# Kernel tuning notes

Measured on AMD Instinct MI355X. Metric: run time of the kernel, lower is better.

Reference implementation:

```python
import jax, jax.numpy as jnp
import numpy as np

N_NODES = 50000
N_EDGES = 1200000
IN_DIM = 128
EDGE_DIM = 64
EMBED_DIM = 64
NUM_HEADS = 8


def segment_softmax(logits, segment_ids, num_segments):
    # numerically stable softmax over segments (receivers)
    mx = jax.ops.segment_max(logits, segment_ids, num_segments)
    e = jnp.exp(logits - mx[segment_ids])
    denom = jax.ops.segment_sum(e, segment_ids, num_segments)
    return e / denom[segment_ids]


def mish(x):
    return x * jnp.tanh(jax.nn.softplus(x))


def setup_inputs() -> dict:
    key = jax.random.key(0)
    ks = jax.random.split(key, 8)
    node_features = jax.random.normal(ks[0], (N_NODES, IN_DIM), dtype=jnp.float32)
    edge_features = jax.random.normal(ks[1], (N_EDGES, EDGE_DIM), dtype=jnp.float32)
    global_features = jax.random.normal(ks[2], (32,), dtype=jnp.float32)
    senders = jax.random.randint(ks[3], (N_EDGES,), 0, N_NODES, dtype=jnp.int32)
    receivers = jax.random.randint(ks[4], (N_EDGES,), 0, N_NODES, dtype=jnp.int32)
    W_kernel = jax.random.normal(ks[5], (IN_DIM, EMBED_DIM), dtype=jnp.float32) * (2.0 / (IN_DIM + EMBED_DIM)) ** 0.5
    W_bias = jnp.zeros((EMBED_DIM,), dtype=jnp.float32)
    We_kernel = jax.random.normal(ks[6], (EDGE_DIM, EMBED_DIM), dtype=jnp.float32) * (2.0 / (EDGE_DIM + EMBED_DIM)) ** 0.5
    We_bias = jnp.zeros((EMBED_DIM,), dtype=jnp.float32)
    a = jax.random.normal(ks[7], (NUM_HEADS, EMBED_DIM // NUM_HEADS), dtype=jnp.float32) * (2.0 / (NUM_HEADS + EMBED_DIM // NUM_HEADS)) ** 0.5
    return dict(node_features=node_features, edge_features=edge_features,
                global_features=global_features, senders=senders, receivers=receivers,
                W_kernel=W_kernel, W_bias=W_bias, We_kernel=We_kernel, We_bias=We_bias, a=a)


def reference(node_features, edge_features, global_features, senders, receivers,
              W_kernel, W_bias, We_kernel, We_bias, a):
    num_nodes = node_features.shape[0]
    H, D = a.shape  # num_heads, head_dim
    # share_weights=True: one Dense projects nodes for both send and recv roles
    nodes = node_features @ W_kernel + W_bias            # [N, H*D]
    send_edges = nodes[senders]                          # [E, H*D] gather
    recv_edges = nodes[receivers]                        # [E, H*D] gather
    x = send_edges + recv_edges + (edge_features @ We_kernel + We_bias)
    x = mish(x)
    xh = x.reshape(-1, H, D)                             # [E, H, D]
    attn_logits = jnp.sum(xh * a, axis=-1, keepdims=True)  # [E, H, 1]
    attn_weights = segment_softmax(attn_logits, receivers, num_nodes)  # [E, H, 1]
    edges = attn_weights * send_edges.reshape(-1, H, D)  # [E, H, D]
    edges = edges.reshape(-1, H * D)
    new_nodes = jax.ops.segment_sum(edges, receivers, num_nodes)  # [N, H*D]
    return new_nodes
```

## Files before the change

kernel.cpp:

```cpp
#include <hip/hip_runtime.h>
#include <math.h>

#define IN_DIM   128
#define EDGE_DIM 64
#define ED       64
#define NH       8
#define CAP      64
#define NPB      512

typedef __attribute__((ext_vector_type(8))) __bf16 bf16x8;
typedef __attribute__((ext_vector_type(4))) __bf16 bf16x4;
typedef __attribute__((ext_vector_type(4))) float  f32x4;

__device__ __forceinline__ int atomInc(int* p) {
    return __hip_atomic_fetch_add(p, 1, __ATOMIC_RELAXED, __HIP_MEMORY_SCOPE_AGENT);
}

__device__ __forceinline__ float mish_f(float x) {
    float u  = __expf(fminf(x, 15.f));
    float nn = u * (u + 2.f);
    return x * __fdividef(nn, nn + 2.f);
}


__global__ __launch_bounds__(256) void front_k(const float* __restrict__ nf,
                        const float* __restrict__ W,
                        const float* __restrict__ Wb,
                        __bf16* __restrict__ nodes_pf,
                        const int* __restrict__ rcv,
                        const int* __restrict__ snd,
                        int* __restrict__ deg,
                        int2* __restrict__ buck,
                        int nN, int nE, int nbk) {
    if (blockIdx.x >= NPB) {
        int i0 = (blockIdx.x - NPB) * 256 + threadIdx.x;
        int stride = nbk * 256;
        for (int i = i0; i < nE; i += stride) {
            int r = rcv[i];
            int slot = atomInc(&deg[r]);
            if (slot < CAP) buck[(long)r * CAP + slot] = make_int2(i, snd[i]);
        }
        return;
    }
    int lane = threadIdx.x & 63;
    int col  = lane & 15;
    int q    = lane >> 4;
    int wid    = blockIdx.x * 4 + (threadIdx.x >> 6);
    int nwaves = NPB * 4;

    bf16x8 aw[4][4];
#pragma unroll
    for (int c = 0; c < 4; c++)
#pragma unroll
        for (int s = 0; s < 4; s++)
#pragma unroll
            for (int i = 0; i < 8; i++)
                aw[c][s][i] = (__bf16)W[(s * 32 + q * 8 + i) * ED + c * 16 + col];
    f32x4 wbv[4];
#pragma unroll
    for (int c = 0; c < 4; c++)
#pragma unroll
        for (int r = 0; r < 4; r++)
            wbv[c][r] = Wb[c * 16 + q * 4 + r];

    int ngroups = (nN + 15) >> 4;
    for (int g = wid; g < ngroups; g += nwaves) {
        int n = g * 16 + col;
        bool valid = (n < nN);
        long nb = (long)(valid ? n : nN - 1) * IN_DIM;
        bf16x8 bfr[4];
#pragma unroll
        for (int s = 0; s < 4; s++) {
            float4 f0 = *(const float4*)(nf + nb + s * 32 + q * 8);
            float4 f1 = *(const float4*)(nf + nb + s * 32 + q * 8 + 4);
            bfr[s][0] = (__bf16)f0.x; bfr[s][1] = (__bf16)f0.y;
            bfr[s][2] = (__bf16)f0.z; bfr[s][3] = (__bf16)f0.w;
            bfr[s][4] = (__bf16)f1.x; bfr[s][5] = (__bf16)f1.y;
            bfr[s][6] = (__bf16)f1.z; bfr[s][7] = (__bf16)f1.w;
        }
        f32x4 acc[4];
#pragma unroll
        for (int c = 0; c < 4; c++) {
            acc[c] = wbv[c];
#pragma unroll
            for (int s = 0; s < 4; s++)
                acc[c] = __builtin_amdgcn_mfma_f32_16x16x32_bf16(aw[c][s], bfr[s], acc[c], 0, 0, 0);
        }
        if (valid) {
            bf16x8 v01, v23;
#pragma unroll
            for (int i = 0; i < 8; i++) {
                v01[i] = (__bf16)acc[i >> 2][i & 3];
                v23[i] = (__bf16)acc[2 + (i >> 2)][i & 3];
            }
            *(bf16x8*)(nodes_pf + (long)n * ED + q * 16)     = v01;
            *(bf16x8*)(nodes_pf + (long)n * ED + q * 16 + 8) = v23;
        }
    }
}

__global__ __launch_bounds__(256) void gemm_pass1(
                           const float* __restrict__ ef,
                           const int* __restrict__ snd,
                           const int* __restrict__ rcv,
                           const __bf16* __restrict__ nodes_pf,
                           const float* __restrict__ We,
                           const float* __restrict__ Web,
                           const float* __restrict__ a,
                           __bf16* __restrict__ w8, int nE) {
    int lane = threadIdx.x & 63;
    int col  = lane & 15;
    int q    = lane >> 4;
    int wid    = blockIdx.x * (blockDim.x >> 6) + (threadIdx.x >> 6);
    int nwaves = gridDim.x * (blockDim.x >> 6);

    bf16x8 aw[4][2];
#pragma unroll
    for (int c = 0; c < 4; c++)
#pragma unroll
        for (int s = 0; s < 2; s++)
#pragma unroll
            for (int i = 0; i < 8; i++)
                aw[c][s][i] = (__bf16)We[(s * 32 + q * 8 + i) * ED + c * 16 + col];
    f32x4 wbv[4];
    float ahat[4][4];
#pragma unroll
    for (int c = 0; c < 4; c++)
#pragma unroll
        for (int r = 0; r < 4; r++) {
            int j = c * 16 + q * 4 + r;
            wbv[c][r]  = Web[j];
            ahat[c][r] = a[j];
        }

    int ngroups = (nE + 15) >> 4;
    for (int g = wid; g < ngroups; g += nwaves) {
        int e = g * 16 + col;
        bool valid = (e < nE);
        int ec = valid ? e : nE - 1;
        long eb = (long)ec * EDGE_DIM;
        bf16x8 bfr[2];
#pragma unroll
        for (int s = 0; s < 2; s++) {
            f32x4 f0 = __builtin_nontemporal_load((const f32x4*)(ef + eb + s * 32 + q * 8));
            f32x4 f1 = __builtin_nontemporal_load((const f32x4*)(ef + eb + s * 32 + q * 8 + 4));
            bfr[s][0] = (__bf16)f0[0]; bfr[s][1] = (__bf16)f0[1];
            bfr[s][2] = (__bf16)f0[2]; bfr[s][3] = (__bf16)f0[3];
            bfr[s][4] = (__bf16)f1[0]; bfr[s][5] = (__bf16)f1[1];
            bfr[s][6] = (__bf16)f1[2]; bfr[s][7] = (__bf16)f1[3];
        }
        int se = snd[ec], re = rcv[ec];
        bf16x8 s01 = *(const bf16x8*)(nodes_pf + (long)se * ED + q * 16);
        bf16x8 s23 = *(const bf16x8*)(nodes_pf + (long)se * ED + q * 16 + 8);
        bf16x8 r01 = *(const bf16x8*)(nodes_pf + (long)re * ED + q * 16);
        bf16x8 r23 = *(const bf16x8*)(nodes_pf + (long)re * ED + q * 16 + 8);

        f32x4 acc[4];
#pragma unroll
        for (int c = 0; c < 4; c++) {
            acc[c] = wbv[c];
            acc[c] = __builtin_amdgcn_mfma_f32_16x16x32_bf16(aw[c][0], bfr[0], acc[c], 0, 0, 0);
            acc[c] = __builtin_amdgcn_mfma_f32_16x16x32_bf16(aw[c][1], bfr[1], acc[c], 0, 0, 0);
        }
        float p[4];
#pragma unroll
        for (int c = 0; c < 4; c++) {
            float ph = 0.f;
#pragma unroll
            for (int r = 0; r < 4; r++) {
                float sv = (c < 2) ? (float)s01[c * 4 + r] : (float)s23[(c - 2) * 4 + r];
                float rv = (c < 2) ? (float)r01[c * 4 + r] : (float)r23[(c - 2) * 4 + r];
                float x = acc[c][r] + sv + rv;
                ph = fmaf(mish_f(x), ahat[c][r], ph);
            }
            p[c] = ph;
        }
        float w[4];
#pragma unroll
        for (int c = 0; c < 4; c++) {
            p[c] += __shfl_xor(p[c], 16);
            w[c] = __expf(p[c]);
        }
        if (valid) {
            if (q == 0) {
                bf16x4 v;
#pragma unroll
                for (int c = 0; c < 4; c++) v[c] = (__bf16)w[c];
                *(bf16x4*)(w8 + (long)e * NH) = v;
            } else if (q == 2) {
                bf16x4 v;
#pragma unroll
                for (int c = 0; c < 4; c++) v[c] = (__bf16)w[c];
                *(bf16x4*)(w8 + (long)e * NH + 4) = v;
            }
        }
    }
}

__global__ __launch_bounds__(256) void seg_sum(const int* __restrict__ deg,
                        const int2* __restrict__ buck,
                        const __bf16* __restrict__ w8,
                        const __bf16* __restrict__ nodes_pf,
                        float* __restrict__ out, int nN) {
    int rn = blockIdx.x * 4 + (threadIdx.x >> 6);
    if (rn >= nN) return;
    int j = threadIdx.x & 63;
    int qq = j >> 4, cc = (j >> 2) & 3, rr = j & 3;
    int f = cc * 16 + qq * 4 + rr;
    int h = f >> 3;
    int widx = (h & 1) * 4 + (h >> 1);
    int dg = min(deg[rn], CAP);
    long base = (long)rn * CAP;
    float acc = 0.f, dn = 0.f;
    for (int s0 = 0; s0 < dg; s0 += 4) {
        int2 b[4];
#pragma unroll
        for (int k = 0; k < 4; k++)
            b[k] = buck[base + min(s0 + k, dg - 1)];
        float wv[4], sv[4];
#pragma unroll
        for (int k = 0; k < 4; k++) {
            bool v = (s0 + k) < dg;
            wv[k] = v ? (float)w8[(long)b[k].x * NH + widx] : 0.f;
            sv[k] = (float)nodes_pf[(long)b[k].y * ED + j];
        }
#pragma unroll
        for (int k = 0; k < 4; k++) {
            acc = fmaf(wv[k], sv[k], acc);
            dn += wv[k];
        }
    }
    out[(long)rn * ED + f] = (dn > 0.f) ? __fdividef(acc, dn) : 0.f;
}

extern "C" void kernel_launch(void* const* d_in, const int* in_sizes, int n_in,
                              void* d_out, int out_size, void* d_ws, size_t ws_size,
                              hipStream_t stream) {
    const float* nf  = (const float*)d_in[0];
    const float* ef  = (const float*)d_in[1];
    const int*   snd = (const int*)d_in[3];
    const int*   rcv = (const int*)d_in[4];
    const float* W   = (const float*)d_in[5];
    const float* Wb  = (const float*)d_in[6];
    const float* We  = (const float*)d_in[7];
    const float* Web = (const float*)d_in[8];
    const float* a   = (const float*)d_in[9];

    int nN = in_sizes[0] / IN_DIM;
    int nE = in_sizes[3];
    float* out = (float*)d_out;

    __bf16* nodes_pf = (__bf16*)d_ws;
    __bf16* w8       = nodes_pf + (size_t)nN * ED;
    int*    deg      = (int*)(w8 + (size_t)nE * NH);
    int2*   buck     = (int2*)(deg + nN);

    hipMemsetAsync(deg, 0, (size_t)nN * sizeof(int), stream);

    int nbk = 1536;
    front_k<<<NPB + nbk, 256, 0, stream>>>(nf, W, Wb, nodes_pf,
                                           rcv, snd, deg, buck, nN, nE, nbk);
    gemm_pass1<<<2048, 256, 0, stream>>>(ef, snd, rcv, nodes_pf, We, Web, a,
                                         w8, nE);
    seg_sum<<<(nN + 3) / 4, 256, 0, stream>>>(deg, buck, w8, nodes_pf, out, nN);
}
```

Before: 294.3 us.

## Move edge bucketing into edge GEMM kernel and widen seg_sum gather batch

Bucketing of edges by receiver now runs in dedicated blocks of the edge-GEMM kernel instead of alongside the node projection, so the atomic-heavy scatter overlaps the larger, bandwidth-bound edge pass. The node projection becomes its own small kernel. seg_sum now loads 8 bucket entries per iteration instead of 4 to expose more memory-level parallelism. The trade-off is that the heavy kernel's bucket blocks compete with the GEMM blocks for bandwidth and CU slots, and the wider gather raises register pressure and adds wasted clamped loads for low-degree nodes.

```diff
diff --git a/kernel.cpp b/kernel.cpp
--- a/kernel.cpp
+++ b/kernel.cpp
@@ -6,7 +6,8 @@
 #define ED       64
 #define NH       8
 #define CAP      64
-#define NPB      512
+#define BKB      512
+#define GMB      2048
 
 typedef __attribute__((ext_vector_type(8))) __bf16 bf16x8;
 typedef __attribute__((ext_vector_type(4))) __bf16 bf16x4;
@@ -23,30 +24,15 @@
 }
 
 
-__global__ __launch_bounds__(256) void front_k(const float* __restrict__ nf,
-                        const float* __restrict__ W,
-                        const float* __restrict__ Wb,
-                        __bf16* __restrict__ nodes_pf,
-                        const int* __restrict__ rcv,
-                        const int* __restrict__ snd,
-                        int* __restrict__ deg,
-                        int2* __restrict__ buck,
-                        int nN, int nE, int nbk) {
-    if (blockIdx.x >= NPB) {
-        int i0 = (blockIdx.x - NPB) * 256 + threadIdx.x;
-        int stride = nbk * 256;
-        for (int i = i0; i < nE; i += stride) {
-            int r = rcv[i];
-            int slot = atomInc(&deg[r]);
-            if (slot < CAP) buck[(long)r * CAP + slot] = make_int2(i, snd[i]);
-        }
-        return;
-    }
+__global__ __launch_bounds__(256) void node_proj(const float* __restrict__ nf,
+                          const float* __restrict__ W,
+                          const float* __restrict__ Wb,
+                          __bf16* __restrict__ nodes_pf, int nN) {
     int lane = threadIdx.x & 63;
     int col  = lane & 15;
     int q    = lane >> 4;
     int wid    = blockIdx.x * 4 + (threadIdx.x >> 6);
-    int nwaves = NPB * 4;
+    int nwaves = gridDim.x * 4;
 
     bf16x8 aw[4][4];
 #pragma unroll
@@ -99,7 +85,7 @@
     }
 }
 
-__global__ __launch_bounds__(256) void gemm_pass1(
+__global__ __launch_bounds__(256) void gemm_bucket(
                            const float* __restrict__ ef,
                            const int* __restrict__ snd,
                            const int* __restrict__ rcv,
@@ -107,12 +93,23 @@
                            const float* __restrict__ We,
                            const float* __restrict__ Web,
                            const float* __restrict__ a,
-                           __bf16* __restrict__ w8, int nE) {
+                           __bf16* __restrict__ w8,
+                           int* __restrict__ deg,
+                           int2* __restrict__ buck, int nE) {
+    if (blockIdx.x < BKB) {
+        int i0 = blockIdx.x * 256 + threadIdx.x;
+        for (int i = i0; i < nE; i += BKB * 256) {
+            int r = rcv[i];
+            int slot = atomInc(&deg[r]);
+            if (slot < CAP) buck[(long)r * CAP + slot] = make_int2(i, snd[i]);
+        }
+        return;
+    }
     int lane = threadIdx.x & 63;
     int col  = lane & 15;
     int q    = lane >> 4;
-    int wid    = blockIdx.x * (blockDim.x >> 6) + (threadIdx.x >> 6);
-    int nwaves = gridDim.x * (blockDim.x >> 6);
+    int wid    = (blockIdx.x - BKB) * 4 + (threadIdx.x >> 6);
+    int nwaves = GMB * 4;
 
     bf16x8 aw[4][2];
 #pragma unroll
@@ -212,20 +209,20 @@
     int dg = min(deg[rn], CAP);
     long base = (long)rn * CAP;
     float acc = 0.f, dn = 0.f;
-    for (int s0 = 0; s0 < dg; s0 += 4) {
-        int2 b[4];
-#pragma unroll
-        for (int k = 0; k < 4; k++)
+    for (int s0 = 0; s0 < dg; s0 += 8) {
+        int2 b[8];
+#pragma unroll
+        for (int k = 0; k < 8; k++)
             b[k] = buck[base + min(s0 + k, dg - 1)];
-        float wv[4], sv[4];
-#pragma unroll
-        for (int k = 0; k < 4; k++) {
+        float wv[8], sv[8];
+#pragma unroll
+        for (int k = 0; k < 8; k++) {
             bool v = (s0 + k) < dg;
             wv[k] = v ? (float)w8[(long)b[k].x * NH + widx] : 0.f;
             sv[k] = (float)nodes_pf[(long)b[k].y * ED + j];
         }
 #pragma unroll
-        for (int k = 0; k < 4; k++) {
+        for (int k = 0; k < 8; k++) {
             acc = fmaf(wv[k], sv[k], acc);
             dn += wv[k];
         }
@@ -257,10 +254,8 @@
 
     hipMemsetAsync(deg, 0, (size_t)nN * sizeof(int), stream);
 
-    int nbk = 1536;
-    front_k<<<NPB + nbk, 256, 0, stream>>>(nf, W, Wb, nodes_pf,
-                                           rcv, snd, deg, buck, nN, nE, nbk);
-    gemm_pass1<<<2048, 256, 0, stream>>>(ef, snd, rcv, nodes_pf, We, Web, a,
-                                         w8, nE);
+    node_proj<<<512, 256, 0, stream>>>(nf, W, Wb, nodes_pf, nN);
+    gemm_bucket<<<BKB + GMB, 256, 0, stream>>>(ef, snd, rcv, nodes_pf, We, Web, a,
+                                               w8, deg, buck, nE);
     seg_sum<<<(nN + 3) / 4, 256, 0, stream>>>(deg, buck, w8, nodes_pf, out, nN);
 }
```

Result: faster. 275.4 us (median of 2 runs) (-6.4%).
